# Performance work log

Measured on AMD Instinct MI355X. Metric: run time of the kernel, lower is better.

Reference implementation:

```python
import jax, jax.numpy as jnp
import numpy as np

# dims
B, L = 2, 1024            # batch, seq len (queries == keys)
DQ, DK, DSRC = 1024, 1024, 512
VIEWS, WIDTH, TOPK = 8, 4, 8
DVP = DQ // VIEWS         # per-view head dim = 128
PAD_F = (WIDTH - 1) // 2  # dilocal 'same' zero padding (stride=1, dilation=1)
PAD_B = (WIDTH - 1) - PAD_F


def setup_inputs() -> dict:
    key = jax.random.key(0)
    ks = jax.random.split(key, 5)
    s = 0.02
    return {
        "query": jax.random.normal(ks[0], (B, L, DQ), jnp.float32),
        "key_t": jax.random.normal(ks[1], (B, L, DK), jnp.float32),
        "source": jax.random.normal(ks[2], (B, L, DSRC), jnp.float32),
        "wq": jax.random.normal(ks[3], (VIEWS, DVP, DQ), jnp.float32) * s,
        "bq": jnp.zeros((VIEWS, DVP), jnp.float32),
        "wk": jax.random.normal(ks[4], (VIEWS, DVP, DK), jnp.float32) * s,
        "bk": jnp.zeros((VIEWS, DVP), jnp.float32),
    }


def reference(query, key_t, source, wq, bq, wk, bk):
    # --- ViewPointFactory.forward ---
    # multi-view projections: [B, L, D] -> [B, views, L, dvp]
    q = jnp.einsum('bld,vkd->bvlk', query, wq) + bq[None, :, None, :]
    k = jnp.einsum('bld,vkd->bvlk', key_t, wk) + bk[None, :, None, :]
    # attention scores over all keys: [B, views, Lq, Lk] (no sqrt(d) scaling in source)
    score = jnp.einsum('bvqd,bvkd->bvqk', q, k)
    # torch.sort(descending) + slice == top_k with sorted values
    vals, idx = jax.lax.top_k(score, TOPK)          # [B, views, Lq, TOPK]
    weights = jax.nn.softmax(vals, axis=-1)

    # --- ViewPoint.__call__(source) ---
    # dilocal: width-WIDTH local windows, stride 1, dilation 1, zero 'same' pad
    padded = jnp.pad(source, ((0, 0), (PAD_F, PAD_B), (0, 0)))
    win_idx = jnp.arange(L)[:, None] + jnp.arange(WIDTH)[None, :]  # [L, WIDTH]
    windows = padded[:, win_idx, :]                 # [B, L, WIDTH, DSRC]

    # gather the top-k key windows per (view, query): [B, views, Lq, TOPK, WIDTH, DSRC]
    gathered = jax.vmap(lambda w, i: w[i])(windows, idx)
    # weighted sum over top-k -> [B, views, Lq, WIDTH, DSRC]
    out = jnp.einsum('bvqk,bvqkwd->bvqwd', weights, gathered)
    return out
```

## Files before the change

### kernel.cpp

```cpp
#include <hip/hip_runtime.h>
#include <cstdint>

#define L_SEQ 1024
#define DSRC 512
#define XPL 2097152L
#define WPL 1048576L

typedef __attribute__((ext_vector_type(8))) short short8;
typedef __attribute__((ext_vector_type(4))) float floatx4;

__device__ __forceinline__ unsigned short f2bf(float f) {
  unsigned int x = __float_as_uint(f);
  x += 0x7fff + ((x >> 16) & 1);
  return (unsigned short)(x >> 16);
}
__device__ __forceinline__ float bf2f(unsigned short h) {
  return __uint_as_float((unsigned)h << 16);
}
__device__ __forceinline__ void split3(float f, unsigned short* h) {
  h[0] = f2bf(f);
  float d = f - bf2f(h[0]);
  h[1] = f2bf(d);
  h[2] = f2bf(d - bf2f(h[1]));
}

__device__ __forceinline__ void gload_lds16(const void* g, void* l) {
  __builtin_amdgcn_global_load_lds(
      (const __attribute__((address_space(1))) unsigned int*)g,
      (__attribute__((address_space(3))) unsigned int*)l, 16, 0, 0);
}

__device__ __forceinline__ bool better(float av, int ac, float bv, int bc) {
  return av > bv || (av == bv && ac < bc);
}
__device__ __forceinline__ void ins8(float (&tv)[8], int (&ti)[8], float v, int c) {
  if (better(v, c, tv[7], ti[7])) {
    tv[7] = v; ti[7] = c;
#pragma unroll
    for (int s = 7; s > 0; s--)
      if (better(tv[s], ti[s], tv[s - 1], ti[s - 1])) {
        float a = tv[s]; tv[s] = tv[s - 1]; tv[s - 1] = a;
        int b2 = ti[s]; ti[s] = ti[s - 1]; ti[s - 1] = b2;
      }
  }
}
__device__ __forceinline__ void quadmerge_store(float (&tv)[8], int (&ti)[8],
                                                float* Mv, int* Mi, int base, int quad) {
#pragma unroll
  for (int t = 0; t < 8; t++) {
    float bv = tv[0]; int bc = ti[0];
    float ov = __shfl_xor(bv, 16); int oc = __shfl_xor(bc, 16);
    if (better(ov, oc, bv, bc)) { bv = ov; bc = oc; }
    ov = __shfl_xor(bv, 32); oc = __shfl_xor(bc, 32);
    if (better(ov, oc, bv, bc)) { bv = ov; bc = oc; }
    if (bc == ti[0]) {
#pragma unroll
      for (int s = 0; s < 7; s++) { tv[s] = tv[s + 1]; ti[s] = ti[s + 1]; }
      tv[7] = -1e30f; ti[7] = 0x7FFFFFFF;
    }
    if (quad == 0) { Mv[base + t] = bv; Mi[base + t] = bc; }
  }
}

__global__ __launch_bounds__(256) void split_inputs_k(
    const float* __restrict__ query, const float* __restrict__ key_t,
    const float* __restrict__ wq, const float* __restrict__ wk,
    ushort* __restrict__ xs, ushort* __restrict__ wsp) {
  int blk = blockIdx.x;
  const float* in; ushort* out; long pl; int idx;
  if (blk < 2048)      { in = query; out = xs;           pl = XPL; idx = blk; }
  else if (blk < 4096) { in = key_t; out = xs + 3 * XPL; pl = XPL; idx = blk - 2048; }
  else if (blk < 5120) { in = wq;    out = wsp;          pl = WPL; idx = blk - 4096; }
  else                 { in = wk;    out = wsp + 3 * WPL; pl = WPL; idx = blk - 5120; }
  long e = (long)idx * 1024 + threadIdx.x * 4;
  float4 v = *(const float4*)(in + e);
  unsigned short h0[3], h1[3], h2[3], h3[3];
  split3(v.x, h0); split3(v.y, h1); split3(v.z, h2); split3(v.w, h3);
#pragma unroll
  for (int s = 0; s < 3; s++) {
    ushort4 u; u.x = h0[s]; u.y = h1[s]; u.z = h2[s]; u.w = h3[s];
    *(ushort4*)(out + s * pl + e) = u;
  }
}

__global__ __launch_bounds__(512, 2) void proj_gemm_k(
    const ushort* __restrict__ xs, const ushort* __restrict__ wsp,
    ushort* __restrict__ qs, ushort* __restrict__ ks,
    const float* __restrict__ bq, const float* __restrict__ bk) {
  __shared__ ushort As[2][3][4096];
  __shared__ ushort Bs[2][3][4096];
  int z = blockIdx.z;
  const ushort* Ab = xs + (long)z * 3 * XPL + (long)blockIdx.y * 128 * 1024;
  const ushort* Bb = wsp + (long)z * 3 * WPL + (long)blockIdx.x * 128 * 1024;

  int tid = threadIdx.x;
  int lane = tid & 63, wv = tid >> 6;
  int wm = wv >> 2, wn = wv & 3;
  int quad = lane >> 4, l16 = lane & 15;

  int sr = tid >> 2;
  int scq = (((tid & 3) ^ ((sr >> 1) & 3)) << 3);

  floatx4 acc[4][2] = {};

#pragma unroll
  for (int s = 0; s < 3; s++) {
    gload_lds16(Ab + (long)s * XPL + (long)sr * 1024 + scq, &As[0][s][wv * 512]);
    gload_lds16(Bb + (long)s * WPL + (long)sr * 1024 + scq, &Bs[0][s][wv * 512]);
  }
  __syncthreads();

  int cur = 0;
#pragma unroll 2
  for (int t = 0; t < 32; t++) {
    if (t < 31) {
      int k0 = (t + 1) * 32;
#pragma unroll
      for (int s = 0; s < 3; s++) {
        gload_lds16(Ab + (long)s * XPL + (long)sr * 1024 + k0 + scq, &As[cur ^ 1][s][wv * 512]);
        gload_lds16(Bb + (long)s * WPL + (long)sr * 1024 + k0 + scq, &Bs[cur ^ 1][s][wv * 512]);
      }
    }
    short8 af[3][4];
#pragma unroll
    for (int s = 0; s < 3; s++)
#pragma unroll
      for (int i = 0; i < 4; i++) {
        int row = wm * 64 + i * 16 + l16;
        int qa = (quad ^ ((row >> 1) & 3)) << 3;
        af[s][i] = *(const short8*)(&As[cur][s][row * 32 + qa]);
      }
#pragma unroll
    for (int j = 0; j < 2; j++) {
      int rowb = wn * 32 + j * 16 + l16;
      int boff = rowb * 32 + ((quad ^ ((rowb >> 1) & 3)) << 3);
      short8 b0 = *(const short8*)(&Bs[cur][0][boff]);
      short8 b1 = *(const short8*)(&Bs[cur][1][boff]);
      short8 b2 = *(const short8*)(&Bs[cur][2][boff]);
#pragma unroll
      for (int i = 0; i < 4; i++) {
        acc[i][j] = __builtin_amdgcn_mfma_f32_16x16x32_bf16(af[1][i], b1, acc[i][j], 0, 0, 0);
        acc[i][j] = __builtin_amdgcn_mfma_f32_16x16x32_bf16(af[0][i], b2, acc[i][j], 0, 0, 0);
        acc[i][j] = __builtin_amdgcn_mfma_f32_16x16x32_bf16(af[2][i], b0, acc[i][j], 0, 0, 0);
        acc[i][j] = __builtin_amdgcn_mfma_f32_16x16x32_bf16(af[0][i], b1, acc[i][j], 0, 0, 0);
        acc[i][j] = __builtin_amdgcn_mfma_f32_16x16x32_bf16(af[1][i], b0, acc[i][j], 0, 0, 0);
        acc[i][j] = __builtin_amdgcn_mfma_f32_16x16x32_bf16(af[0][i], b0, acc[i][j], 0, 0, 0);
      }
    }
    __syncthreads();
    cur ^= 1;
  }

  ushort* Ob = z ? ks : qs;
  const float* bias = z ? bk : bq;
#pragma unroll
  for (int j = 0; j < 2; j++) {
    int col = blockIdx.x * 128 + wn * 32 + j * 16 + l16;
    float bv = bias[col];
#pragma unroll
    for (int i = 0; i < 4; i++) {
#pragma unroll
      for (int r = 0; r < 4; r++) {
        long row = blockIdx.y * 128 + wm * 64 + i * 16 + quad * 4 + r;
        float val = acc[i][j][r] + bv;
        unsigned short h[3]; split3(val, h);
        long e = row * 1024 + col;
#pragma unroll
        for (int s = 0; s < 3; s++) Ob[s * XPL + e] = h[s];
      }
    }
  }
}

__global__ __launch_bounds__(512, 2) void score_topk_k(
    const ushort* __restrict__ qs, const ushort* __restrict__ ks,
    float* __restrict__ wts, int* __restrict__ idxs) {
  __shared__ __align__(16) ushort smem[49152];
  ushort* Qsm = smem;
  ushort* Kb0 = smem + 24576;
  float* Mv = (float*)(smem + 24576);
  int*   Mi = (int*)(smem + 24576 + 4096);

  int fid = blockIdx.x + 16 * (blockIdx.y + 8 * blockIdx.z);
  int xcd = fid & 7, jj = fid >> 3;
  int pair = xcd * 2 + (jj & 1);
  int rt = jj >> 1;
  int v = pair & 7, b = pair >> 3;

  const long arow0 = (long)b * 1024 + rt * 64;
  const long brow0 = (long)b * 1024;
  const int vb = v * 128;

  int tid = threadIdx.x;
  int lane = tid & 63, wv = tid >> 6;
  int kg = wv & 3, qg = wv >> 2;
  int quad = lane >> 4, l16 = lane & 15;

#pragma unroll
  for (int n = 0; n < 6; n++) {
    int base = n * 512 + wv * 64;
    int sl = base + lane;
    int s = sl >> 10, rem = sl & 1023;
    int r = rem >> 4, sq = rem & 15;
    int qb = sq ^ (r & 7);
    gload_lds16(qs + (long)s * XPL + (arow0 + r) * 1024 + vb + qb * 8,
                &Qsm[base * 8]);
  }

  auto stageK = [&](int step, int bsel) {
    int ct2 = step >> 2, kk2 = step & 3;
    long kb = brow0 + ct2 * 128;
    int k0 = kk2 * 32;
    ushort* Kd = Kb0 + bsel * 12288;
#pragma unroll
    for (int n = 0; n < 3; n++) {
      int base = n * 512 + wv * 64;
      int sl = base + lane;
      int s = sl >> 9, rem = sl & 511;
      int c = rem >> 2, sq = rem & 3;
      int qb = sq ^ ((c >> 1) & 3);
      gload_lds16(ks + (long)s * XPL + (kb + c) * 1024 + vb + k0 + qb * 8,
                  &Kd[base * 8]);
    }
  };

  stageK(0, 0);
  __syncthreads();

  floatx4 acc[2][2] = {};
  float tv0[8], tv1[8]; int ti0[8], ti1[8];
#pragma unroll
  for (int t = 0; t < 8; t++) {
    tv0[t] = tv1[t] = -1e30f; ti0[t] = ti1[t] = 0x7FFFFFFF;
  }

  int buf = 0;
  for (int ct = 0; ct < 8; ct++) {
#pragma unroll
    for (int kk = 0; kk < 4; kk++) {
      int step = ct * 4 + kk;
      if (step < 31) stageK(step + 1, buf ^ 1);

      const ushort* Kc = Kb0 + buf * 12288;
      short8 qf[3][2], kf[3][2];
#pragma unroll
      for (int s = 0; s < 3; s++)
#pragma unroll
        for (int j = 0; j < 2; j++) {
          int q = qg * 32 + j * 16 + l16;
          int sqa = (kk * 4 + quad) ^ (q & 7);
          qf[s][j] = *(const short8*)(&Qsm[s * 8192 + q * 128 + sqa * 8]);
        }
#pragma unroll
      for (int s = 0; s < 3; s++)
#pragma unroll
        for (int i = 0; i < 2; i++) {
          int c = kg * 32 + i * 16 + l16;
          int sqb = quad ^ ((c >> 1) & 3);
          kf[s][i] = *(const short8*)(&Kc[s * 4096 + c * 32 + sqb * 8]);
        }
#pragma unroll
      for (int j = 0; j < 2; j++)
#pragma unroll
        for (int i = 0; i < 2; i++) {
          acc[i][j] = __builtin_amdgcn_mfma_f32_16x16x32_bf16(kf[1][i], qf[1][j], acc[i][j], 0, 0, 0);
          acc[i][j] = __builtin_amdgcn_mfma_f32_16x16x32_bf16(kf[2][i], qf[0][j], acc[i][j], 0, 0, 0);
          acc[i][j] = __builtin_amdgcn_mfma_f32_16x16x32_bf16(kf[0][i], qf[2][j], acc[i][j], 0, 0, 0);
          acc[i][j] = __builtin_amdgcn_mfma_f32_16x16x32_bf16(kf[1][i], qf[0][j], acc[i][j], 0, 0, 0);
          acc[i][j] = __builtin_amdgcn_mfma_f32_16x16x32_bf16(kf[0][i], qf[1][j], acc[i][j], 0, 0, 0);
          acc[i][j] = __builtin_amdgcn_mfma_f32_16x16x32_bf16(kf[0][i], qf[0][j], acc[i][j], 0, 0, 0);
        }
      __syncthreads();
      buf ^= 1;
    }

#pragma unroll
    for (int i = 0; i < 2; i++)
#pragma unroll
      for (int r = 0; r < 4; r++) {
        int kglob = ct * 128 + kg * 32 + i * 16 + quad * 4 + r;
        ins8(tv0, ti0, acc[i][0][r], kglob);
        ins8(tv1, ti1, acc[i][1][r], kglob);
        acc[i][0][r] = 0.0f; acc[i][1][r] = 0.0f;
      }
  }

  int q0 = qg * 32 + l16;
  quadmerge_store(tv0, ti0, Mv, Mi, (kg * 64 + q0) * 8, quad);
  int q1 = q0 + 16;
  quadmerge_store(tv1, ti1, Mv, Mi, (kg * 64 + q1) * 8, quad);
  __syncthreads();

  if (tid < 64) {
    int q = tid;
    int i0 = 0, i1 = 0, i2 = 0, i3 = 0;
    float pv[8]; int pc[8];
#pragma unroll
    for (int t = 0; t < 8; t++) {
      float v0 = Mv[(0 * 64 + q) * 8 + i0]; int c0 = Mi[(0 * 64 + q) * 8 + i0];
      float v1 = Mv[(1 * 64 + q) * 8 + i1]; int c1 = Mi[(1 * 64 + q) * 8 + i1];
      float v2 = Mv[(2 * 64 + q) * 8 + i2]; int c2 = Mi[(2 * 64 + q) * 8 + i2];
      float v3 = Mv[(3 * 64 + q) * 8 + i3]; int c3 = Mi[(3 * 64 + q) * 8 + i3];
      bool b01 = better(v1, c1, v0, c0);
      float w01v = b01 ? v1 : v0; int w01c = b01 ? c1 : c0; int w01l = b01 ? 1 : 0;
      bool b23 = better(v3, c3, v2, c2);
      float w23v = b23 ? v3 : v2; int w23c = b23 ? c3 : c2; int w23l = b23 ? 3 : 2;
      bool bf_ = better(w23v, w23c, w01v, w01c);
      float wvv = bf_ ? w23v : w01v; int wcc = bf_ ? w23c : w01c;
      int wl = bf_ ? w23l : w01l;
      i0 += (wl == 0); i1 += (wl == 1); i2 += (wl == 2); i3 += (wl == 3);
      pv[t] = wvv; pc[t] = wcc;
    }
    float m = pv[0], sum = 0.f, e[8];
#pragma unroll
    for (int t = 0; t < 8; t++) { e[t] = __expf(pv[t] - m); sum += e[t]; }
    float inv = 1.0f / sum;
    long grow = (long)b * 8192 + v * 1024 + rt * 64 + q;
#pragma unroll
    for (int t = 0; t < 8; t++) {
      wts[grow * 8 + t] = e[t] * inv;
      idxs[grow * 8 + t] = pc[t];
    }
  }
}

__global__ __launch_bounds__(256) void gather_out_k(const float* __restrict__ src,
                                                    const float* __restrict__ wts,
                                                    const int* __restrict__ idxs,
                                                    float* __restrict__ out) {
  int rowid = blockIdx.x;
  int b = rowid >> 13;
  int tid = threadIdx.x;
  int d4 = tid & 127;
  int w0 = (tid >> 7) << 1;
  const float4* s4 = (const float4*)src + (long)b * (L_SEQ * (DSRC / 4));
  float wt[8]; int id[8];
#pragma unroll
  for (int k = 0; k < 8; k++) {
    wt[k] = wts[(long)rowid * 8 + k];
    id[k] = idxs[(long)rowid * 8 + k];
  }
  float ax = 0, ay = 0, az = 0, aw = 0;
  float bx = 0, by = 0, bz2 = 0, bw = 0;
#pragma unroll
  for (int k = 0; k < 8; k++) {
    int r0 = id[k] + w0 - 1;
    if ((unsigned)r0 < (unsigned)L_SEQ) {
      float4 x = s4[(long)r0 * 128 + d4];
      ax += wt[k] * x.x; ay += wt[k] * x.y; az += wt[k] * x.z; aw += wt[k] * x.w;
    }
    int r1 = r0 + 1;
    if ((unsigned)r1 < (unsigned)L_SEQ) {
      float4 x = s4[(long)r1 * 128 + d4];
      bx += wt[k] * x.x; by += wt[k] * x.y; bz2 += wt[k] * x.z; bw += wt[k] * x.w;
    }
  }
  float4* o4 = (float4*)out + ((long)rowid * 4 + w0) * 128 + d4;
  o4[0] = make_float4(ax, ay, az, aw);
  o4[128] = make_float4(bx, by, bz2, bw);
}

extern "C" void kernel_launch(void* const* d_in, const int* in_sizes, int n_in,
                              void* d_out, int out_size, void* d_ws, size_t ws_size,
                              hipStream_t stream) {
  (void)in_sizes; (void)n_in; (void)out_size; (void)ws_size;
  const float* query  = (const float*)d_in[0];
  const float* key_t  = (const float*)d_in[1];
  const float* source = (const float*)d_in[2];
  const float* wq     = (const float*)d_in[3];
  const float* bq     = (const float*)d_in[4];
  const float* wk     = (const float*)d_in[5];
  const float* bk     = (const float*)d_in[6];

  char* ws = (char*)d_ws;
  ushort* qs  = (ushort*)(ws);
  ushort* ksp = (ushort*)(ws + 12582912);
  float*  wts = (float*)(ws + 25165824);
  int*    idxs= (int*)(ws + 25690112);
  ushort* xs  = (ushort*)(ws + 26214400);
  ushort* wsp = (ushort*)(ws + 51380224);

  split_inputs_k<<<6144, 256, 0, stream>>>(query, key_t, wq, wk, xs, wsp);
  proj_gemm_k<<<dim3(8, 16, 2), 512, 0, stream>>>(xs, wsp, qs, ksp, bq, bk);
  score_topk_k<<<dim3(16, 8, 2), 512, 0, stream>>>(qs, ksp, wts, idxs);
  gather_out_k<<<16384, 256, 0, stream>>>(source, wts, idxs, (float*)d_out);
}
```

Measured before the change: 323.0 us.

## Halve score tile rows, raise occupancy, defer top-k inserts into MFMA loop

The score/top-k kernel now handles 32 query rows per block instead of 64, doubling the grid, shrinking LDS and targeting 4 blocks per CU. The top-k insertion for the previous column tile is spread across the next tile's k-steps so it can overlap with MFMA work, and it uses a branch-free compare-swap without index tie-breaking. K-staging addresses are precomputed once. The trade-off is that K tiles are reloaded twice as often across blocks, and ties between equal scores may now be ordered differently than before.

Measured after the change: 289.8 us. -10.3%, faster.

```diff
diff --git a/kernel.cpp b/kernel.cpp
--- a/kernel.cpp
+++ b/kernel.cpp
@@ -33,15 +33,17 @@
 __device__ __forceinline__ bool better(float av, int ac, float bv, int bc) {
   return av > bv || (av == bv && ac < bc);
 }
-__device__ __forceinline__ void ins8(float (&tv)[8], int (&ti)[8], float v, int c) {
-  if (better(v, c, tv[7], ti[7])) {
+__device__ __forceinline__ void ins8f(float (&tv)[8], int (&ti)[8], float v, int c) {
+  if (v > tv[7]) {
     tv[7] = v; ti[7] = c;
 #pragma unroll
-    for (int s = 7; s > 0; s--)
-      if (better(tv[s], ti[s], tv[s - 1], ti[s - 1])) {
-        float a = tv[s]; tv[s] = tv[s - 1]; tv[s - 1] = a;
-        int b2 = ti[s]; ti[s] = ti[s - 1]; ti[s - 1] = b2;
-      }
+    for (int s = 7; s > 0; s--) {
+      float x = tv[s], y = tv[s - 1];
+      int xi = ti[s], yi = ti[s - 1];
+      bool sw = x > y;
+      tv[s] = sw ? y : x;     tv[s - 1] = sw ? x : y;
+      ti[s] = sw ? yi : xi;   ti[s - 1] = sw ? xi : yi;
+    }
   }
 }
 __device__ __forceinline__ void quadmerge_store(float (&tv)[8], int (&ti)[8],
@@ -172,22 +174,22 @@
   }
 }
 
-__global__ __launch_bounds__(512, 2) void score_topk_k(
+__global__ __launch_bounds__(512, 4) void score_topk_k(
     const ushort* __restrict__ qs, const ushort* __restrict__ ks,
     float* __restrict__ wts, int* __restrict__ idxs) {
-  __shared__ __align__(16) ushort smem[49152];
+  __shared__ __align__(16) ushort smem[36864];
   ushort* Qsm = smem;
-  ushort* Kb0 = smem + 24576;
-  float* Mv = (float*)(smem + 24576);
-  int*   Mi = (int*)(smem + 24576 + 4096);
-
-  int fid = blockIdx.x + 16 * (blockIdx.y + 8 * blockIdx.z);
+  ushort* Kb0 = smem + 12288;
+  float* Mv = (float*)(smem + 12288);
+  int*   Mi = (int*)(smem + 12288 + 4096);
+
+  int fid = blockIdx.x + 32 * (blockIdx.y + 8 * blockIdx.z);
   int xcd = fid & 7, jj = fid >> 3;
   int pair = xcd * 2 + (jj & 1);
   int rt = jj >> 1;
   int v = pair & 7, b = pair >> 3;
 
-  const long arow0 = (long)b * 1024 + rt * 64;
+  const long arow0 = (long)b * 1024 + rt * 32;
   const long brow0 = (long)b * 1024;
   const int vb = v * 128;
 
@@ -197,42 +199,44 @@
   int quad = lane >> 4, l16 = lane & 15;
 
 #pragma unroll
-  for (int n = 0; n < 6; n++) {
+  for (int n = 0; n < 3; n++) {
     int base = n * 512 + wv * 64;
     int sl = base + lane;
-    int s = sl >> 10, rem = sl & 1023;
+    int s = sl >> 9, rem = sl & 511;
     int r = rem >> 4, sq = rem & 15;
     int qb = sq ^ (r & 7);
     gload_lds16(qs + (long)s * XPL + (arow0 + r) * 1024 + vb + qb * 8,
                 &Qsm[base * 8]);
   }
 
+  const ushort* gKp[3]; int ldsKo[3];
+#pragma unroll
+  for (int n = 0; n < 3; n++) {
+    int base = n * 512 + wv * 64;
+    int sl = base + lane;
+    int s = sl >> 9, rem = sl & 511;
+    int c = rem >> 2, sq = rem & 3;
+    int qb = sq ^ ((c >> 1) & 3);
+    gKp[n] = ks + (long)s * XPL + (brow0 + c) * 1024 + vb + qb * 8;
+    ldsKo[n] = base * 8;
+  }
   auto stageK = [&](int step, int bsel) {
-    int ct2 = step >> 2, kk2 = step & 3;
-    long kb = brow0 + ct2 * 128;
-    int k0 = kk2 * 32;
+    long off = (long)(step >> 2) * 131072 + (step & 3) * 32;
     ushort* Kd = Kb0 + bsel * 12288;
 #pragma unroll
-    for (int n = 0; n < 3; n++) {
-      int base = n * 512 + wv * 64;
-      int sl = base + lane;
-      int s = sl >> 9, rem = sl & 511;
-      int c = rem >> 2, sq = rem & 3;
-      int qb = sq ^ ((c >> 1) & 3);
-      gload_lds16(ks + (long)s * XPL + (kb + c) * 1024 + vb + k0 + qb * 8,
-                  &Kd[base * 8]);
-    }
+    for (int n = 0; n < 3; n++)
+      gload_lds16(gKp[n] + off, &Kd[ldsKo[n]]);
   };
 
   stageK(0, 0);
   __syncthreads();
 
-  floatx4 acc[2][2] = {};
-  float tv0[8], tv1[8]; int ti0[8], ti1[8];
-#pragma unroll
-  for (int t = 0; t < 8; t++) {
-    tv0[t] = tv1[t] = -1e30f; ti0[t] = ti1[t] = 0x7FFFFFFF;
-  }
+  floatx4 acc[2] = {};
+  float tv[8]; int ti[8];
+#pragma unroll
+  for (int t = 0; t < 8; t++) { tv[t] = -1e30f; ti[t] = 0x7FFFFFFF; }
+  float pend[8];
+  int pbase = 0;
 
   int buf = 0;
   for (int ct = 0; ct < 8; ct++) {
@@ -242,15 +246,13 @@
       if (step < 31) stageK(step + 1, buf ^ 1);
 
       const ushort* Kc = Kb0 + buf * 12288;
-      short8 qf[3][2], kf[3][2];
-#pragma unroll
-      for (int s = 0; s < 3; s++)
-#pragma unroll
-        for (int j = 0; j < 2; j++) {
-          int q = qg * 32 + j * 16 + l16;
-          int sqa = (kk * 4 + quad) ^ (q & 7);
-          qf[s][j] = *(const short8*)(&Qsm[s * 8192 + q * 128 + sqa * 8]);
-        }
+      short8 qf[3], kf[3][2];
+#pragma unroll
+      for (int s = 0; s < 3; s++) {
+        int q = qg * 16 + l16;
+        int sqa = (kk * 4 + quad) ^ (q & 7);
+        qf[s] = *(const short8*)(&Qsm[s * 4096 + q * 128 + sqa * 8]);
+      }
 #pragma unroll
       for (int s = 0; s < 3; s++)
 #pragma unroll
@@ -260,47 +262,50 @@
           kf[s][i] = *(const short8*)(&Kc[s * 4096 + c * 32 + sqb * 8]);
         }
 #pragma unroll
-      for (int j = 0; j < 2; j++)
-#pragma unroll
-        for (int i = 0; i < 2; i++) {
-          acc[i][j] = __builtin_amdgcn_mfma_f32_16x16x32_bf16(kf[1][i], qf[1][j], acc[i][j], 0, 0, 0);
-          acc[i][j] = __builtin_amdgcn_mfma_f32_16x16x32_bf16(kf[2][i], qf[0][j], acc[i][j], 0, 0, 0);
-          acc[i][j] = __builtin_amdgcn_mfma_f32_16x16x32_bf16(kf[0][i], qf[2][j], acc[i][j], 0, 0, 0);
-          acc[i][j] = __builtin_amdgcn_mfma_f32_16x16x32_bf16(kf[1][i], qf[0][j], acc[i][j], 0, 0, 0);
-          acc[i][j] = __builtin_amdgcn_mfma_f32_16x16x32_bf16(kf[0][i], qf[1][j], acc[i][j], 0, 0, 0);
-          acc[i][j] = __builtin_amdgcn_mfma_f32_16x16x32_bf16(kf[0][i], qf[0][j], acc[i][j], 0, 0, 0);
-        }
+      for (int i = 0; i < 2; i++) {
+        acc[i] = __builtin_amdgcn_mfma_f32_16x16x32_bf16(kf[1][i], qf[1], acc[i], 0, 0, 0);
+        acc[i] = __builtin_amdgcn_mfma_f32_16x16x32_bf16(kf[2][i], qf[0], acc[i], 0, 0, 0);
+        acc[i] = __builtin_amdgcn_mfma_f32_16x16x32_bf16(kf[0][i], qf[2], acc[i], 0, 0, 0);
+        acc[i] = __builtin_amdgcn_mfma_f32_16x16x32_bf16(kf[1][i], qf[0], acc[i], 0, 0, 0);
+        acc[i] = __builtin_amdgcn_mfma_f32_16x16x32_bf16(kf[0][i], qf[1], acc[i], 0, 0, 0);
+        acc[i] = __builtin_amdgcn_mfma_f32_16x16x32_bf16(kf[0][i], qf[0], acc[i], 0, 0, 0);
+      }
+
+      if (ct > 0) {
+        const int t0 = kk * 2, t1 = kk * 2 + 1;
+        ins8f(tv, ti, pend[t0], pbase + ((t0 >> 2) << 4) + (quad << 2) + (t0 & 3));
+        ins8f(tv, ti, pend[t1], pbase + ((t1 >> 2) << 4) + (quad << 2) + (t1 & 3));
+      }
       __syncthreads();
       buf ^= 1;
     }
-
 #pragma unroll
     for (int i = 0; i < 2; i++)
 #pragma unroll
       for (int r = 0; r < 4; r++) {
-        int kglob = ct * 128 + kg * 32 + i * 16 + quad * 4 + r;
-        ins8(tv0, ti0, acc[i][0][r], kglob);
-        ins8(tv1, ti1, acc[i][1][r], kglob);
-        acc[i][0][r] = 0.0f; acc[i][1][r] = 0.0f;
-      }
-  }
-
-  int q0 = qg * 32 + l16;
-  quadmerge_store(tv0, ti0, Mv, Mi, (kg * 64 + q0) * 8, quad);
-  int q1 = q0 + 16;
-  quadmerge_store(tv1, ti1, Mv, Mi, (kg * 64 + q1) * 8, quad);
+        pend[i * 4 + r] = acc[i][r];
+        acc[i][r] = 0.0f;
+      }
+    pbase = ct * 128 + kg * 32;
+  }
+#pragma unroll
+  for (int t = 0; t < 8; t++)
+    ins8f(tv, ti, pend[t], pbase + ((t >> 2) << 4) + (quad << 2) + (t & 3));
+
+  int row = qg * 16 + l16;
+  quadmerge_store(tv, ti, Mv, Mi, (kg * 32 + row) * 8, quad);
   __syncthreads();
 
-  if (tid < 64) {
+  if (tid < 32) {
     int q = tid;
     int i0 = 0, i1 = 0, i2 = 0, i3 = 0;
     float pv[8]; int pc[8];
 #pragma unroll
     for (int t = 0; t < 8; t++) {
-      float v0 = Mv[(0 * 64 + q) * 8 + i0]; int c0 = Mi[(0 * 64 + q) * 8 + i0];
-      float v1 = Mv[(1 * 64 + q) * 8 + i1]; int c1 = Mi[(1 * 64 + q) * 8 + i1];
-      float v2 = Mv[(2 * 64 + q) * 8 + i2]; int c2 = Mi[(2 * 64 + q) * 8 + i2];
-      float v3 = Mv[(3 * 64 + q) * 8 + i3]; int c3 = Mi[(3 * 64 + q) * 8 + i3];
+      float v0 = Mv[(0 * 32 + q) * 8 + i0]; int c0 = Mi[(0 * 32 + q) * 8 + i0];
+      float v1 = Mv[(1 * 32 + q) * 8 + i1]; int c1 = Mi[(1 * 32 + q) * 8 + i1];
+      float v2 = Mv[(2 * 32 + q) * 8 + i2]; int c2 = Mi[(2 * 32 + q) * 8 + i2];
+      float v3 = Mv[(3 * 32 + q) * 8 + i3]; int c3 = Mi[(3 * 32 + q) * 8 + i3];
       bool b01 = better(v1, c1, v0, c0);
       float w01v = b01 ? v1 : v0; int w01c = b01 ? c1 : c0; int w01l = b01 ? 1 : 0;
       bool b23 = better(v3, c3, v2, c2);
@@ -315,7 +320,7 @@
 #pragma unroll
     for (int t = 0; t < 8; t++) { e[t] = __expf(pv[t] - m); sum += e[t]; }
     float inv = 1.0f / sum;
-    long grow = (long)b * 8192 + v * 1024 + rt * 64 + q;
+    long grow = (long)b * 8192 + v * 1024 + rt * 32 + q;
 #pragma unroll
     for (int t = 0; t < 8; t++) {
       wts[grow * 8 + t] = e[t] * inv;
@@ -382,6 +387,6 @@
 
   split_inputs_k<<<6144, 256, 0, stream>>>(query, key_t, wq, wk, xs, wsp);
   proj_gemm_k<<<dim3(8, 16, 2), 512, 0, stream>>>(xs, wsp, qs, ksp, bq, bk);
-  score_topk_k<<<dim3(16, 8, 2), 512, 0, stream>>>(qs, ksp, wts, idxs);
+  score_topk_k<<<dim3(32, 8, 2), 512, 0, stream>>>(qs, ksp, wts, idxs);
   gather_out_k<<<16384, 256, 0, stream>>>(source, wts, idxs, (float*)d_out);
 }
```
